# Optimization experiments

Measured on AMD Instinct MI355X. Metric: run time of the kernel, lower is better.

The kernel has to match this reference:

```python
import jax, jax.numpy as jnp
import numpy as np

TOPK = 64  # init kwarg: number of dst routes kept per src node


def setup_inputs() -> dict:
    key = jax.random.key(0)
    ks = jax.random.split(key, 6)
    B, J, K, D, Dd = 4, 4096, 8192, 64, 64  # batch, src_nodes, dst_nodes, src_dim, dst_dim
    val = jax.random.normal(ks[0], (B, J, D), jnp.float32)
    state = jax.random.normal(ks[1], (B, J), jnp.float32)
    dst_state = jax.random.normal(ks[2], (B, K), jnp.float32)
    dst_val = jax.random.normal(ks[3], (B, K, Dd), jnp.float32)
    W_route = jax.random.normal(ks[4], (D, K), jnp.float32) / np.sqrt(D).astype(np.float32)
    W_val = jax.random.normal(ks[5], (D, Dd), jnp.float32) / np.sqrt(D).astype(np.float32)
    return dict(val=val, state=state, dst_state=dst_state, dst_val=dst_val,
                W_route=W_route, W_val=W_val)


def _sparse_routes(logits, topk):
    # top-k indices per src node, scatter a bool mask, masked softmax over dst axis
    _, idx = jax.lax.top_k(logits, topk)              # [B, J, topk]
    B, J, K = logits.shape
    mask = jnp.zeros((B, J, K), dtype=bool)
    mask = mask.at[jnp.arange(B)[:, None, None],
                   jnp.arange(J)[None, :, None], idx].set(True)
    neg = jnp.finfo(logits.dtype).min
    return jax.nn.softmax(jnp.where(mask, logits, neg), axis=-1)


def reference(val, state, dst_state, dst_val, W_route, W_val):
    # route_fn: linear over src val -> logits [B, J, K]
    logits = jnp.einsum('bjd,dk->bjk', val, W_route)
    routes = _sparse_routes(logits, TOPK)             # sparse masked softmax
    projected_val = jnp.einsum('bjd,de->bje', val, W_val)  # val_proj_fn (Linear)
    projected_state = state                            # state_proj_fn = Identity
    sender = jax.nn.softplus(state)                    # state_activation_fn
    weighted = routes * sender[..., None]              # [B, J, K]
    delta_state = jnp.einsum('bjk,bj->bk', weighted, projected_state)
    delta_val = jnp.einsum('bjk,bjd->bkd', weighted, projected_val)
    # merge_mode='add'
    return (dst_state + delta_state, dst_val + delta_val)
```

## Files before the change

### kernel.cpp

```cpp
#include <hip/hip_runtime.h>
#include <math.h>

#define NB 4
#define J 4096
#define KDIM 8192
#define DDIM 64
#define DD 64
#define TOPK 64

#define BM 32
#define THREADS 512
#define THREADS_SEL 256
#define NITER_H 8
#define CAP_H 128
#define GCAP 256
#define OVFCAP 262144

#define KG 128
#define NGRP (KDIM / KG)
#define GLCAP 8192
#define BINROWS 16
#define BINCAP 96
#define CH 128
#define MAXTASK 40960

typedef _Float16 half8_t __attribute__((ext_vector_type(8)));
typedef float f32x16 __attribute__((ext_vector_type(16)));
union H8 { half8_t h; uint4 u; };
__device__ __forceinline__ half8_t as_h8(uint4 v) { H8 x; x.u = v; return x.h; }

__device__ __forceinline__ unsigned f2key(float f) {
  unsigned u = __float_as_uint(f);
  return u ^ (unsigned)(((int)u >> 31) | 0x80000000);
}
__device__ __forceinline__ float key2f(unsigned k) {
  unsigned u = (k & 0x80000000u) ? (k & 0x7FFFFFFFu) : ~k;
  return __uint_as_float(u);
}
__device__ __forceinline__ unsigned wred_maxu(unsigned v) {
  #pragma unroll
  for (int o = 32; o > 0; o >>= 1) { unsigned u = __shfl_xor(v, o, 64); v = u > v ? u : v; }
  return v;
}
__device__ __forceinline__ unsigned wred_minu(unsigned v) {
  #pragma unroll
  for (int o = 32; o > 0; o >>= 1) { unsigned u = __shfl_xor(v, o, 64); v = u < v ? u : v; }
  return v;
}
__device__ __forceinline__ float wred_addf(float v) {
  #pragma unroll
  for (int o = 32; o > 0; o >>= 1) v += __shfl_xor(v, o, 64);
  return v;
}

__global__ void k_prep(const float* __restrict__ W, unsigned* __restrict__ WFh,
                       float* __restrict__ WT)
{
  __shared__ _Float16 lh[64][64];
  __shared__ float lf[64][64];
  const int t = threadIdx.x;
  const int kb = blockIdx.x * 64;
  for (int i = t; i < 4096; i += 256) {
    const int d = i >> 6, c = i & 63;
    const float x = W[(size_t)d * KDIM + kb + c];
    lh[c][d] = (_Float16)x;
    lf[c][d] = x;
  }
  __syncthreads();
  for (int q = t; q < 512; q += 256) {
    const int gt2 = q >> 8, rem = q & 255;
    const int ks = rem >> 6, lane = rem & 63;
    const int c = gt2 * 32 + (lane & 31);
    const int d0 = ks * 16 + (lane >> 5) * 8;
    const int gtile = blockIdx.x * 2 + gt2;
    const size_t off = ((size_t)(gtile * 4 + ks) * 64 + lane) * 4;
    *(uint4*)(WFh + off) = *(const uint4*)&lh[c][d0];
  }
  for (int q = t; q < 1024; q += 256) {
    const int c = q >> 4, d0 = (q & 15) * 4;
    *(float4*)(WT + (size_t)(kb + c) * DDIM + d0) = *(const float4*)&lf[c][d0];
  }
}

__global__ void k_init(const float* __restrict__ dst_state,
                       const float* __restrict__ dst_val,
                       float* __restrict__ out_state, float* __restrict__ out_val)
{
  const size_t i = (size_t)blockIdx.x * blockDim.x + threadIdx.x;
  const size_t stride = (size_t)gridDim.x * blockDim.x;
  const size_t nS = (size_t)NB * KDIM;
  const size_t nV4 = (size_t)NB * KDIM * DD / 4;
  for (size_t q = i; q < nV4; q += stride)
    ((float4*)out_val)[q] = ((const float4*)dst_val)[q];
  for (size_t q = i; q < nS; q += stride)
    out_state[q] = dst_state[q];
}

__global__ __launch_bounds__(THREADS, 4) void k_cand(
    const float* __restrict__ val, const unsigned* __restrict__ WFh,
    const float* __restrict__ W_val, float* __restrict__ pv,
    unsigned short* __restrict__ gidx, unsigned* __restrict__ gcnt,
    float* __restrict__ gtau, unsigned* __restrict__ flags)
{
  __shared__ __align__(16) float val_lds[BM][DDIM + 4];
  __shared__ unsigned short cand_idx[BM][CAP_H];
  __shared__ unsigned have[BM];
  __shared__ float tauF[BM];

  const int t = threadIdx.x;
  const int lane = t & 63;
  const int wv = t >> 6;
  const int hi = lane >> 5;
  const int lane31 = lane & 31;
  const int row0 = blockIdx.x * BM;
  const int h = blockIdx.y;

  {
    const int r = t >> 4, d0 = (t & 15) * 4;
    const float4 v4 = *(const float4*)(val + (size_t)(row0 + r) * DDIM + d0);
    val_lds[r][d0] = v4.x; val_lds[r][d0 + 1] = v4.y;
    val_lds[r][d0 + 2] = v4.z; val_lds[r][d0 + 3] = v4.w;
  }
  __syncthreads();

  if (t < BM) {
    float n2 = 0.f;
    #pragma unroll
    for (int d = 0; d < DDIM; ++d) { const float x = val_lds[t][d]; n2 = fmaf(x, x, n2); }
    tauF[t] = 0.26f * sqrtf(n2);
    have[t] = 0u;
    if (h == 0) gtau[row0 + t] = tauF[t];
  }

  half8_t ah[4];
  {
    const int m = lane31;
    #pragma unroll
    for (int ks = 0; ks < 4; ++ks) {
      const int d0 = ks * 16 + hi * 8;
      #pragma unroll
      for (int j = 0; j < 8; ++j) ah[ks][j] = (_Float16)val_lds[m][d0 + j];
    }
  }
  __syncthreads();

  float taufr[16];
  #pragma unroll
  for (int r = 0; r < 16; ++r) taufr[r] = tauF[(r & 3) + 8 * (r >> 2) + 4 * hi];

  const unsigned* wpBase = WFh + (size_t)(h * 128 + wv * 2) * 1024 + lane * 4;
  const unsigned* wp = wpBase;
  uint4 b0 = *(const uint4*)(wp);        uint4 b1 = *(const uint4*)(wp + 256);
  uint4 b2 = *(const uint4*)(wp + 512);  uint4 b3 = *(const uint4*)(wp + 768);
  uint4 b4 = *(const uint4*)(wp + 1024); uint4 b5 = *(const uint4*)(wp + 1280);
  uint4 b6 = *(const uint4*)(wp + 1536); uint4 b7 = *(const uint4*)(wp + 1792);

  #pragma unroll 1
  for (int it = 0; it < NITER_H; ++it) {
    f32x16 acc0, acc1;
    #pragma unroll
    for (int i = 0; i < 16; ++i) { acc0[i] = 0.f; acc1[i] = 0.f; }
    acc0 = __builtin_amdgcn_mfma_f32_32x32x16_f16(ah[0], as_h8(b0), acc0, 0, 0, 0);
    acc1 = __builtin_amdgcn_mfma_f32_32x32x16_f16(ah[0], as_h8(b4), acc1, 0, 0, 0);
    acc0 = __builtin_amdgcn_mfma_f32_32x32x16_f16(ah[1], as_h8(b1), acc0, 0, 0, 0);
    acc1 = __builtin_amdgcn_mfma_f32_32x32x16_f16(ah[1], as_h8(b5), acc1, 0, 0, 0);
    acc0 = __builtin_amdgcn_mfma_f32_32x32x16_f16(ah[2], as_h8(b2), acc0, 0, 0, 0);
    acc1 = __builtin_amdgcn_mfma_f32_32x32x16_f16(ah[2], as_h8(b6), acc1, 0, 0, 0);
    acc0 = __builtin_amdgcn_mfma_f32_32x32x16_f16(ah[3], as_h8(b3), acc0, 0, 0, 0);
    acc1 = __builtin_amdgcn_mfma_f32_32x32x16_f16(ah[3], as_h8(b7), acc1, 0, 0, 0);

    const unsigned colbase = (unsigned)((h * 128 + it * 16 + wv * 2) * 32 + lane31);

    wp = (it == NITER_H - 1) ? wpBase : wp + 16384;
    b0 = *(const uint4*)(wp);        b1 = *(const uint4*)(wp + 256);
    b2 = *(const uint4*)(wp + 512);  b3 = *(const uint4*)(wp + 768);
    b4 = *(const uint4*)(wp + 1024); b5 = *(const uint4*)(wp + 1280);
    b6 = *(const uint4*)(wp + 1536); b7 = *(const uint4*)(wp + 1792);

    #pragma unroll
    for (int r = 0; r < 16; ++r) {
      const int row = (r & 3) + 8 * (r >> 2) + 4 * hi;
      const float tf = taufr[r];
      if (acc0[r] > tf) {
        const unsigned slot = atomicAdd(&have[row], 1u);
        if (slot < CAP_H) cand_idx[row][slot] = (unsigned short)colbase;
      }
      if (acc1[r] > tf) {
        const unsigned slot = atomicAdd(&have[row], 1u);
        if (slot < CAP_H) cand_idx[row][slot] = (unsigned short)(colbase + 32);
      }
    }
  }

  if (h == 1) {
    const int r = t >> 4, e0 = (t & 15) * 4;
    float a0 = 0.f, a1 = 0.f, a2 = 0.f, a3 = 0.f;
    #pragma unroll 8
    for (int d = 0; d < DDIM; ++d) {
      const float v = val_lds[r][d];
      const float4 w4 = *(const float4*)(W_val + (size_t)d * DD + e0);
      a0 = fmaf(v, w4.x, a0); a1 = fmaf(v, w4.y, a1);
      a2 = fmaf(v, w4.z, a2); a3 = fmaf(v, w4.w, a3);
    }
    *(float4*)(pv + (size_t)(row0 + r) * DD + e0) = make_float4(a0, a1, a2, a3);
  }

  __syncthreads();

  for (int i = t; i < BM * CAP_H; i += THREADS) {
    const int r = i >> 7, s = i & (CAP_H - 1);
    const unsigned hv = have[r];
    const int lim = hv < CAP_H ? (int)hv : CAP_H;
    if (s < lim)
      gidx[(size_t)(row0 + r) * GCAP + h * CAP_H + s] = cand_idx[r][s];
  }
  if (t < BM) {
    const unsigned hv = have[t];
    gcnt[(size_t)(row0 + t) * 2 + h] = hv < CAP_H ? hv : CAP_H;
    if (hv > CAP_H) flags[row0 + t] = 1u;
  }
}

__global__ __launch_bounds__(THREADS_SEL, 4) void k_select(
    const float* __restrict__ val, const float* __restrict__ state,
    const float* __restrict__ WT,
    const unsigned short* __restrict__ gidx, const unsigned* __restrict__ gcnt,
    const float* __restrict__ gtau, unsigned* __restrict__ flags,
    uint2* __restrict__ routes, unsigned* __restrict__ rcnt)
{
  __shared__ float skey[THREADS_SEL / 64][GCAP];
  const int t = threadIdx.x;
  const int lane = t & 63;
  const int wv = t >> 6;
  const int row = blockIdx.x * (THREADS_SEL / 64) + wv;

  if (flags[row]) return;
  const int c0 = (int)gcnt[(size_t)row * 2];
  const int c1 = (int)gcnt[(size_t)row * 2 + 1];
  const int nc = c0 + c1;
  if (nc < TOPK) { if (lane == 0) flags[row] = 1u; return; }
  const float tau = gtau[row];

  const int cq = lane >> 2;
  const int dq = lane & 3;
  float4 v4[4];
  #pragma unroll
  for (int j = 0; j < 4; ++j)
    v4[j] = *(const float4*)(val + (size_t)row * DDIM + j * 16 + dq * 4);

  const unsigned short* grow = gidx + (size_t)row * GCAP;

  unsigned id4[4];
  #pragma unroll
  for (int i = 0; i < 4; ++i) {
    const int s = i * 64 + lane;
    id4[i] = 0xFFFFFFFFu;
    if (s < nc) {
      const int ps = s < c0 ? s : (s - c0 + CAP_H);
      id4[i] = (unsigned)grow[ps];
    }
  }

  for (int s0 = 0; s0 < nc; s0 += 32) {
    const int sA = s0 + cq;
    const int sB = s0 + 16 + cq;
    const bool okA = sA < nc, okB = sB < nc;
    int psA = sA < c0 ? sA : (sA - c0 + CAP_H); if (!okA) psA = 0;
    int psB = sB < c0 ? sB : (sB - c0 + CAP_H); if (!okB) psB = 0;
    const unsigned kkA = (unsigned)grow[psA] & (KDIM - 1);
    const unsigned kkB = (unsigned)grow[psB] & (KDIM - 1);
    const float* wtA = WT + (size_t)kkA * DDIM + dq * 4;
    const float* wtB = WT + (size_t)kkB * DDIM + dq * 4;
    float4 wA[4], wB[4];
    #pragma unroll
    for (int j = 0; j < 4; ++j) wA[j] = *(const float4*)(wtA + j * 16);
    #pragma unroll
    for (int j = 0; j < 4; ++j) wB[j] = *(const float4*)(wtB + j * 16);
    float aA = 0.f, aB = 0.f;
    #pragma unroll
    for (int j = 0; j < 4; ++j) {
      aA = fmaf(v4[j].x, wA[j].x, aA); aA = fmaf(v4[j].y, wA[j].y, aA);
      aA = fmaf(v4[j].z, wA[j].z, aA); aA = fmaf(v4[j].w, wA[j].w, aA);
      aB = fmaf(v4[j].x, wB[j].x, aB); aB = fmaf(v4[j].y, wB[j].y, aB);
      aB = fmaf(v4[j].z, wB[j].z, aB); aB = fmaf(v4[j].w, wB[j].w, aB);
    }
    aA += __shfl_xor(aA, 1, 64); aA += __shfl_xor(aA, 2, 64);
    aB += __shfl_xor(aB, 1, 64); aB += __shfl_xor(aB, 2, 64);
    if (dq == 0) {
      if (okA) skey[wv][sA] = aA;
      if (okB) skey[wv][sB] = aB;
    }
  }
  asm volatile("s_waitcnt lgkmcnt(0)" ::: "memory");
  __builtin_amdgcn_sched_barrier(0);

  unsigned k4[4];
  #pragma unroll
  for (int i = 0; i < 4; ++i) {
    const int s = i * 64 + lane;
    k4[i] = (s < nc) ? f2key(skey[wv][s]) : 0u;
  }
  unsigned lmax = k4[0];
  #pragma unroll
  for (int i = 1; i < 4; ++i) lmax = k4[i] > lmax ? k4[i] : lmax;
  const unsigned kmaxAll = wred_maxu(lmax);
  unsigned klo = f2key(0.99f * tau); if (klo == 0u) klo = 1u;
  unsigned khi = kmaxAll + 1u;
  auto cge4 = [&](unsigned th) {
    int c = 0;
    #pragma unroll
    for (int i = 0; i < 4; ++i) c += __popcll(__ballot(k4[i] >= th));
    return c;
  };
  int cnt = nc;
  while (cnt != TOPK && khi - klo > 1u) {
    const unsigned mid = klo + ((khi - klo) >> 1);
    const int c = cge4(mid);
    if (c >= TOPK) { klo = mid; cnt = c; } else khi = mid;
  }
  const unsigned thr = klo;
  if (key2f(thr) <= 1.006f * tau) {
    if (lane == 0) flags[row] = 1u;
    return;
  }
  unsigned selmask = 0u;
  if (cnt == TOPK) {
    #pragma unroll
    for (int i = 0; i < 4; ++i) if (k4[i] >= thr) selmask |= 1u << i;
  } else {
    #pragma unroll
    for (int i = 0; i < 4; ++i) if (k4[i] > thr) selmask |= 1u << i;
    int tot = 0;
    #pragma unroll
    for (int i = 0; i < 4; ++i) tot += __popcll(__ballot((selmask >> i) & 1));
    int need = TOPK - tot;
    while (need > 0) {
      unsigned best = 0xFFFFFFFFu; int bi = -1;
      #pragma unroll
      for (int i = 0; i < 4; ++i)
        if (k4[i] == thr && !(selmask & (1u << i)) && id4[i] < best) { best = id4[i]; bi = i; }
      const unsigned g = wred_minu(best);
      if (g == 0xFFFFFFFFu) break;
      if (bi >= 0 && best == g) selmask |= 1u << bi;
      --need;
    }
  }
  const float m = key2f(kmaxAll);
  float p[4]; float lsum = 0.f;
  #pragma unroll
  for (int i = 0; i < 4; ++i) {
    p[i] = 0.f;
    if (selmask & (1u << i)) { p[i] = __expf(key2f(k4[i]) - m); lsum += p[i]; }
  }
  lsum = wred_addf(lsum);
  const float st = state[row];
  const float sender = st > 20.f ? st : log1pf(__expf(st));
  const float scale = sender / lsum;
  const unsigned jloc = (unsigned)(row & (J - 1));

  uint2* rrow = routes + (size_t)row * 64;
  int pre = 0;
  #pragma unroll
  for (int i = 0; i < 4; ++i) {
    const bool sel = (selmask >> i) & 1;
    const unsigned long long mball = __ballot(sel);
    const int off = pre + __popcll(mball & ((1ull << lane) - 1ull));
    if (sel)
      rrow[off] = make_uint2(__float_as_uint(p[i] * scale),
                             (id4[i] << 12) | jloc);
    pre += __popcll(mball);
  }
  if (lane == 0) rcnt[row] = (unsigned)pre;
}

__global__ void k_fix(const float* __restrict__ val, const float* __restrict__ state,
                      const float* __restrict__ W, const unsigned* __restrict__ flags,
                      uint2* __restrict__ routes, unsigned* __restrict__ rcnt)
{
  __shared__ unsigned anyf;
  __shared__ unsigned lsk[64][TOPK + 1];
  __shared__ unsigned short lsi[64][TOPK];
  const int t = threadIdx.x;
  const int row = blockIdx.x * 64 + t;
  if (t == 0) anyf = 0u;
  __syncthreads();
  const unsigned f = flags[row];
  if (f) anyf = 1u;
  __syncthreads();
  if (!anyf) return;
  if (!f) return;

  float v[DDIM];
  #pragma unroll
  for (int d = 0; d < DDIM; ++d) v[d] = val[(size_t)row * DDIM + d];
  int m = 0, worst = 0;
  for (int k = 0; k < KDIM; ++k) {
    float acc = 0.f;
    #pragma unroll 8
    for (int d = 0; d < DDIM; ++d) acc = fmaf(v[d], W[(size_t)d * KDIM + k], acc);
    const unsigned key = f2key(acc);
    if (m < TOPK) {
      lsk[t][m] = key; lsi[t][m] = (unsigned short)k; ++m;
      if (m == TOPK) {
        worst = 0;
        for (int q = 1; q < TOPK; ++q)
          if (lsk[t][q] < lsk[t][worst] ||
              (lsk[t][q] == lsk[t][worst] && lsi[t][q] > lsi[t][worst])) worst = q;
      }
    } else if (key > lsk[t][worst]) {
      lsk[t][worst] = key; lsi[t][worst] = (unsigned short)k;
      worst = 0;
      for (int q = 1; q < TOPK; ++q)
        if (lsk[t][q] < lsk[t][worst] ||
            (lsk[t][q] == lsk[t][worst] && lsi[t][q] > lsi[t][worst])) worst = q;
    }
  }
  unsigned km = lsk[t][0];
  for (int q = 1; q < TOPK; ++q) if (lsk[t][q] > km) km = lsk[t][q];
  const float mx = key2f(km);
  float lsum = 0.f;
  for (int q = 0; q < TOPK; ++q) lsum += __expf(key2f(lsk[t][q]) - mx);
  const float st = state[row];
  const float sender = st > 20.f ? st : log1pf(__expf(st));
  const float scale = sender / lsum;
  const unsigned jloc = (unsigned)(row & (J - 1));
  uint2* rrow = routes + (size_t)row * 64;
  for (int q = 0; q < TOPK; ++q) {
    const float w = __expf(key2f(lsk[t][q]) - mx) * scale;
    rrow[q] = make_uint2(__float_as_uint(w), ((unsigned)lsi[t][q] << 12) | jloc);
  }
  rcnt[row] = TOPK;
}

__global__ __launch_bounds__(256, 2) void k_bin(
    const uint2* __restrict__ routes, const unsigned* __restrict__ rcnt,
    unsigned* __restrict__ glcnt, uint2* __restrict__ glist,
    unsigned* __restrict__ ovf_cnt, uint2* __restrict__ ovf)
{
  __shared__ uint2 bins[NGRP][BINCAP];
  __shared__ unsigned bcnt[NGRP];
  __shared__ unsigned bbase[NGRP];
  const int t = threadIdx.x;
  const int lane = t & 63;
  const int wv = t >> 6;
  const int row0 = blockIdx.x * BINROWS;
  const int b = row0 / J;

  for (int i = t; i < NGRP; i += 256) bcnt[i] = 0u;
  __syncthreads();

  for (int i = t; i < BINROWS * 64; i += 256) {
    const int r = i >> 6, s = i & 63;
    unsigned n = rcnt[row0 + r]; if (n > 64u) n = 64u;
    if (s < (int)n) {
      const uint2 e = routes[(size_t)(row0 + r) * 64 + s];
      const unsigned k = e.y >> 12;
      const unsigned g = k >> 7;
      const unsigned slot = atomicAdd(&bcnt[g], 1u);
      if (slot < BINCAP) bins[g][slot] = e;
      else {
        const unsigned op = atomicAdd(ovf_cnt, 1u);
        if (op < (unsigned)OVFCAP)
          ovf[op] = make_uint2(e.x, (((unsigned)b * KDIM + k) << 12) | (e.y & (J - 1)));
      }
    }
  }
  __syncthreads();

  if (t < NGRP) {
    unsigned c = bcnt[t]; if (c > BINCAP) c = BINCAP;
    bcnt[t] = c;
    bbase[t] = c ? atomicAdd(&glcnt[b * NGRP + t], c) : 0u;
  }
  __syncthreads();

  for (int g = wv * 16; g < wv * 16 + 16; ++g) {
    const unsigned c = bcnt[g];
    const unsigned base = bbase[g];
    uint2* dst = glist + (size_t)(b * NGRP + g) * GLCAP;
    for (unsigned i2 = lane; i2 < c; i2 += 64) {
      const unsigned pos = base + i2;
      const uint2 e = bins[g][i2];
      if (pos < GLCAP) dst[pos] = e;
      else {
        const unsigned k = e.y >> 12;
        const unsigned op = atomicAdd(ovf_cnt, 1u);
        if (op < (unsigned)OVFCAP)
          ovf[op] = make_uint2(e.x, (((unsigned)b * KDIM + k) << 12) | (e.y & (J - 1)));
      }
    }
  }
}

__global__ void k_sort(const unsigned* __restrict__ glcnt, const uint2* __restrict__ glist,
                       uint2* __restrict__ glist2, unsigned* __restrict__ ntask,
                       uint2* __restrict__ tasks)
{
  __shared__ unsigned hist[KG];
  __shared__ unsigned offs[KG];
  __shared__ unsigned cur[KG];
  const int t = threadIdx.x;
  const int b = blockIdx.x >> 6;
  const int g = blockIdx.x & (NGRP - 1);
  unsigned n = glcnt[b * NGRP + g]; if (n > (unsigned)GLCAP) n = (unsigned)GLCAP;
  const uint2* src = glist + (size_t)(b * NGRP + g) * GLCAP;
  uint2* dst = glist2 + (size_t)(b * NGRP + g) * GLCAP;

  for (int i = t; i < KG; i += 256) hist[i] = 0u;
  __syncthreads();
  for (unsigned i = t; i < n; i += 256)
    atomicAdd(&hist[(src[i].y >> 12) & (KG - 1)], 1u);
  __syncthreads();
  if (t < KG) offs[t] = hist[t];
  __syncthreads();
  for (int d = 1; d < KG; d <<= 1) {
    unsigned v = 0u;
    if (t < KG && t >= d) v = offs[t - d];
    __syncthreads();
    if (t < KG) offs[t] += v;
    __syncthreads();
  }
  if (t < KG) {
    const unsigned h = hist[t];
    const unsigned base = offs[t] - h;
    cur[t] = base;
    if (h) {
      const unsigned nt = (h + CH - 1) / CH;
      unsigned tbase = atomicAdd(ntask, nt);
      const unsigned bk = (unsigned)b * KDIM + (unsigned)g * KG + (unsigned)t;
      for (unsigned s = 0; s < nt && tbase + s < (unsigned)MAXTASK; ++s) {
        const unsigned st = base + s * CH;
        unsigned ln = h - s * CH; if (ln > (unsigned)CH) ln = CH;
        tasks[tbase + s] = make_uint2(bk, st | (ln << 16));
      }
    }
  }
  __syncthreads();
  for (unsigned i = t; i < n; i += 256) {
    const uint2 e = src[i];
    const unsigned p = atomicAdd(&cur[(e.y >> 12) & (KG - 1)], 1u);
    dst[p] = e;
  }
}

__global__ void k_gather(const unsigned* __restrict__ ntask,
                         const uint2* __restrict__ tasks,
                         const uint2* __restrict__ glist2,
                         const float* __restrict__ pv, const float* __restrict__ state,
                         float* __restrict__ out_state, float* __restrict__ out_val)
{
  const unsigned wid = ((unsigned)blockIdx.x * blockDim.x + threadIdx.x) >> 6;
  const int lane = threadIdx.x & 63;
  unsigned nt = *ntask; if (nt > (unsigned)MAXTASK) nt = (unsigned)MAXTASK;
  if (wid >= nt) return;
  const uint2 tk = tasks[wid];
  const unsigned bk = tk.x;
  const int b = (int)(bk >> 13);
  const unsigned k = bk & (KDIM - 1);
  const unsigned g = k >> 7;
  const unsigned st = tk.y & 0xFFFFu;
  const unsigned n = tk.y >> 16;
  const size_t jbase = (size_t)b * J;
  const uint2* lst = glist2 + (size_t)((unsigned)b * NGRP + g) * GLCAP + st;

  float a0 = 0.f, a1 = 0.f, a2 = 0.f, a3 = 0.f;
  float s0 = 0.f, s1 = 0.f, s2 = 0.f, s3 = 0.f;
  unsigned i = 0;
  for (; i + 4 <= n; i += 4) {
    const uint2 e0 = lst[i + 0], e1 = lst[i + 1], e2 = lst[i + 2], e3 = lst[i + 3];
    const float w0 = __uint_as_float(e0.x), w1 = __uint_as_float(e1.x);
    const float w2 = __uint_as_float(e2.x), w3 = __uint_as_float(e3.x);
    const unsigned j0 = e0.y & (J - 1), j1 = e1.y & (J - 1);
    const unsigned j2 = e2.y & (J - 1), j3 = e3.y & (J - 1);
    a0 = fmaf(w0, pv[(jbase + j0) * DD + lane], a0);
    a1 = fmaf(w1, pv[(jbase + j1) * DD + lane], a1);
    a2 = fmaf(w2, pv[(jbase + j2) * DD + lane], a2);
    a3 = fmaf(w3, pv[(jbase + j3) * DD + lane], a3);
    s0 = fmaf(w0, state[jbase + j0], s0); s1 = fmaf(w1, state[jbase + j1], s1);
    s2 = fmaf(w2, state[jbase + j2], s2); s3 = fmaf(w3, state[jbase + j3], s3);
  }
  for (; i < n; ++i) {
    const uint2 e = lst[i];
    const float w = __uint_as_float(e.x);
    const unsigned j = e.y & (J - 1);
    a0 = fmaf(w, pv[(jbase + j) * DD + lane], a0);
    s0 = fmaf(w, state[jbase + j], s0);
  }
  atomicAdd(&out_val[(size_t)bk * DD + lane], (a0 + a1) + (a2 + a3));
  if (lane == 0) atomicAdd(&out_state[bk], (s0 + s1) + (s2 + s3));
}

__global__ void k_ovf(const unsigned* __restrict__ ovf_cnt, const uint2* __restrict__ ovf,
                      const float* __restrict__ pv, const float* __restrict__ state,
                      float* __restrict__ out_state, float* __restrict__ out_val)
{
  unsigned n = *ovf_cnt;
  if (n > (unsigned)OVFCAP) n = (unsigned)OVFCAP;
  const unsigned wglob = (blockIdx.x * blockDim.x + threadIdx.x) >> 6;
  const int lane = threadIdx.x & 63;
  const unsigned nw = (gridDim.x * blockDim.x) >> 6;
  for (unsigned i = wglob; i < n; i += nw) {
    const uint2 e = ovf[i];
    const float w = __uint_as_float(e.x);
    const unsigned bk = e.y >> 12;
    const unsigned j = e.y & (J - 1);
    const size_t jg = (size_t)(bk >> 13) * J + j;
    atomicAdd(&out_val[(size_t)bk * DD + lane], w * pv[jg * DD + lane]);
    if (lane == 0) atomicAdd(&out_state[bk], w * state[jg]);
  }
}

extern "C" void kernel_launch(void* const* d_in, const int* in_sizes, int n_in,
                              void* d_out, int out_size, void* d_ws, size_t ws_size,
                              hipStream_t stream)
{
  (void)in_sizes; (void)n_in; (void)out_size; (void)ws_size;
  const float* val       = (const float*)d_in[0];
  const float* state     = (const float*)d_in[1];
  const float* dst_state = (const float*)d_in[2];
  const float* dst_val   = (const float*)d_in[3];
  const float* W_route   = (const float*)d_in[4];
  const float* W_val     = (const float*)d_in[5];
  float* out_state = (float*)d_out;
  float* out_val   = out_state + (size_t)NB * KDIM;

  char* p = (char*)d_ws;
  unsigned* rcnt    = (unsigned*)p;  p += (size_t)NB * J * 4;
  unsigned* flags   = (unsigned*)p;  p += (size_t)NB * J * 4;
  unsigned* ovf_cnt = (unsigned*)p;  p += 256;
  unsigned* gcnt    = (unsigned*)p;  p += (size_t)NB * J * 2 * 4;
  unsigned* glcnt   = (unsigned*)p;  p += (size_t)NB * NGRP * 4;
  uint2* tasks      = (uint2*)p;     p += (size_t)MAXTASK * 8;
  float* pv         = (float*)p;     p += (size_t)NB * J * DD * 4;
  unsigned* WFh     = (unsigned*)p;  p += (size_t)KDIM * DDIM * 2;
  float* WT         = (float*)p;     p += (size_t)KDIM * DDIM * 4;
  float* gtau       = (float*)p;     p += (size_t)NB * J * 4;
  unsigned short* gidx = (unsigned short*)p;
  uint2* glist2     = (uint2*)p;     p += (size_t)NB * J * GCAP * 2;
  uint2* routes     = (uint2*)p;     p += (size_t)NB * J * 64 * 8;
  uint2* glist      = (uint2*)p;     p += (size_t)NB * NGRP * GLCAP * 8;
  uint2* ovf        = (uint2*)p;     p += (size_t)OVFCAP * 8;
  unsigned* ntask   = ovf_cnt + 1;

  hipMemsetAsync(rcnt, 0,
                 (size_t)NB * J * 4 + (size_t)NB * J * 4 + 256 +
                 (size_t)NB * J * 2 * 4 + (size_t)NB * NGRP * 4, stream);

  hipLaunchKernelGGL(k_prep, dim3(KDIM / 64), dim3(256), 0, stream, W_route, WFh, WT);
  hipLaunchKernelGGL(k_init, dim3(1024), dim3(256), 0, stream,
                     dst_state, dst_val, out_state, out_val);
  hipLaunchKernelGGL(k_cand, dim3(NB * J / BM, 2), dim3(THREADS), 0, stream,
                     val, WFh, W_val, pv, gidx, gcnt, gtau, flags);
  hipLaunchKernelGGL(k_select, dim3(NB * J / (THREADS_SEL / 64)), dim3(THREADS_SEL),
                     0, stream, val, state, WT, gidx, gcnt, gtau, flags,
                     routes, rcnt);
  hipLaunchKernelGGL(k_fix, dim3(NB * J / 64), dim3(64), 0, stream,
                     val, state, W_route, flags, routes, rcnt);
  hipLaunchKernelGGL(k_bin, dim3(NB * J / BINROWS), dim3(256), 0, stream,
                     routes, rcnt, glcnt, glist, ovf_cnt, ovf);
  hipLaunchKernelGGL(k_sort, dim3(NB * NGRP), dim3(256), 0, stream,
                     glcnt, glist, glist2, ntask, tasks);
  hipLaunchKernelGGL(k_gather, dim3(MAXTASK / 4), dim3(256), 0, stream,
                     ntask, tasks, glist2, pv, state, out_state, out_val);
  hipLaunchKernelGGL(k_ovf, dim3(256), dim3(256), 0, stream,
                     ovf_cnt, ovf, pv, state, out_state, out_val);
}
```

Baseline: 196.7 us.

## Split candidate search into four K segments and merge init and overflow kernels

The candidate-filtering kernel now splits the destination axis into four segments instead of two. This doubles the number of blocks and halves the per-block iteration count, with a smaller per-segment candidate cap, and select maps candidate slots across the four segments. The output init copy is folded into the weight-prep kernel as extra blocks, and the overflow scatter is merged into the gather kernel, removing two launches. Costs include recomputing the threshold and staging val in twice as many blocks, and extra segment-mapping arithmetic in select. Rows whose candidates overflow the smaller cap fall back to the slow fix path more often.

```diff
diff --git a/kernel.cpp b/kernel.cpp
--- a/kernel.cpp
+++ b/kernel.cpp
@@ -11,9 +11,10 @@
 #define BM 32
 #define THREADS 512
 #define THREADS_SEL 256
-#define NITER_H 8
-#define CAP_H 128
-#define GCAP 256
+#define NSEG 4
+#define NITER_S 4
+#define CAP_S 80
+#define GCAPR (NSEG * CAP_S)
 #define OVFCAP 262144
 
 #define KG 128
@@ -54,8 +55,23 @@
 }
 
 __global__ void k_prep(const float* __restrict__ W, unsigned* __restrict__ WFh,
-                       float* __restrict__ WT)
-{
+                       float* __restrict__ WT,
+                       const float* __restrict__ dst_state,
+                       const float* __restrict__ dst_val,
+                       float* __restrict__ out_state, float* __restrict__ out_val)
+{
+  if (blockIdx.x >= KDIM / 64) {
+    const unsigned bid2 = blockIdx.x - KDIM / 64;
+    const size_t i = (size_t)bid2 * 256 + threadIdx.x;
+    const size_t stride = (size_t)1024 * 256;
+    const size_t nS = (size_t)NB * KDIM;
+    const size_t nV4 = (size_t)NB * KDIM * DD / 4;
+    for (size_t q = i; q < nV4; q += stride)
+      ((float4*)out_val)[q] = ((const float4*)dst_val)[q];
+    for (size_t q = i; q < nS; q += stride)
+      out_state[q] = dst_state[q];
+    return;
+  }
   __shared__ _Float16 lh[64][64];
   __shared__ float lf[64][64];
   const int t = threadIdx.x;
@@ -82,20 +98,6 @@
   }
 }
 
-__global__ void k_init(const float* __restrict__ dst_state,
-                       const float* __restrict__ dst_val,
-                       float* __restrict__ out_state, float* __restrict__ out_val)
-{
-  const size_t i = (size_t)blockIdx.x * blockDim.x + threadIdx.x;
-  const size_t stride = (size_t)gridDim.x * blockDim.x;
-  const size_t nS = (size_t)NB * KDIM;
-  const size_t nV4 = (size_t)NB * KDIM * DD / 4;
-  for (size_t q = i; q < nV4; q += stride)
-    ((float4*)out_val)[q] = ((const float4*)dst_val)[q];
-  for (size_t q = i; q < nS; q += stride)
-    out_state[q] = dst_state[q];
-}
-
 __global__ __launch_bounds__(THREADS, 4) void k_cand(
     const float* __restrict__ val, const unsigned* __restrict__ WFh,
     const float* __restrict__ W_val, float* __restrict__ pv,
@@ -103,7 +105,7 @@
     float* __restrict__ gtau, unsigned* __restrict__ flags)
 {
   __shared__ __align__(16) float val_lds[BM][DDIM + 4];
-  __shared__ unsigned short cand_idx[BM][CAP_H];
+  __shared__ unsigned short cand_idx[BM][CAP_S];
   __shared__ unsigned have[BM];
   __shared__ float tauF[BM];
 
@@ -148,7 +150,7 @@
   #pragma unroll
   for (int r = 0; r < 16; ++r) taufr[r] = tauF[(r & 3) + 8 * (r >> 2) + 4 * hi];
 
-  const unsigned* wpBase = WFh + (size_t)(h * 128 + wv * 2) * 1024 + lane * 4;
+  const unsigned* wpBase = WFh + (size_t)(h * 64 + wv * 2) * 1024 + lane * 4;
   const unsigned* wp = wpBase;
   uint4 b0 = *(const uint4*)(wp);        uint4 b1 = *(const uint4*)(wp + 256);
   uint4 b2 = *(const uint4*)(wp + 512);  uint4 b3 = *(const uint4*)(wp + 768);
@@ -156,7 +158,7 @@
   uint4 b6 = *(const uint4*)(wp + 1536); uint4 b7 = *(const uint4*)(wp + 1792);
 
   #pragma unroll 1
-  for (int it = 0; it < NITER_H; ++it) {
+  for (int it = 0; it < NITER_S; ++it) {
     f32x16 acc0, acc1;
     #pragma unroll
     for (int i = 0; i < 16; ++i) { acc0[i] = 0.f; acc1[i] = 0.f; }
@@ -169,9 +171,9 @@
     acc0 = __builtin_amdgcn_mfma_f32_32x32x16_f16(ah[3], as_h8(b3), acc0, 0, 0, 0);
     acc1 = __builtin_amdgcn_mfma_f32_32x32x16_f16(ah[3], as_h8(b7), acc1, 0, 0, 0);
 
-    const unsigned colbase = (unsigned)((h * 128 + it * 16 + wv * 2) * 32 + lane31);
-
-    wp = (it == NITER_H - 1) ? wpBase : wp + 16384;
+    const unsigned colbase = (unsigned)((h * 64 + it * 16 + wv * 2) * 32 + lane31);
+
+    wp = (it == NITER_S - 1) ? wpBase : wp + 16384;
     b0 = *(const uint4*)(wp);        b1 = *(const uint4*)(wp + 256);
     b2 = *(const uint4*)(wp + 512);  b3 = *(const uint4*)(wp + 768);
     b4 = *(const uint4*)(wp + 1024); b5 = *(const uint4*)(wp + 1280);
@@ -183,16 +185,16 @@
       const float tf = taufr[r];
       if (acc0[r] > tf) {
         const unsigned slot = atomicAdd(&have[row], 1u);
-        if (slot < CAP_H) cand_idx[row][slot] = (unsigned short)colbase;
+        if (slot < CAP_S) cand_idx[row][slot] = (unsigned short)colbase;
       }
       if (acc1[r] > tf) {
         const unsigned slot = atomicAdd(&have[row], 1u);
-        if (slot < CAP_H) cand_idx[row][slot] = (unsigned short)(colbase + 32);
+        if (slot < CAP_S) cand_idx[row][slot] = (unsigned short)(colbase + 32);
       }
     }
   }
 
-  if (h == 1) {
+  if (h == 3) {
     const int r = t >> 4, e0 = (t & 15) * 4;
     float a0 = 0.f, a1 = 0.f, a2 = 0.f, a3 = 0.f;
     #pragma unroll 8
@@ -207,17 +209,18 @@
 
   __syncthreads();
 
-  for (int i = t; i < BM * CAP_H; i += THREADS) {
-    const int r = i >> 7, s = i & (CAP_H - 1);
+  #pragma unroll
+  for (int rr = 0; rr < 4; ++rr) {
+    const int r = wv * 4 + rr;
     const unsigned hv = have[r];
-    const int lim = hv < CAP_H ? (int)hv : CAP_H;
-    if (s < lim)
-      gidx[(size_t)(row0 + r) * GCAP + h * CAP_H + s] = cand_idx[r][s];
+    const int lim = hv < CAP_S ? (int)hv : CAP_S;
+    for (int s = lane; s < lim; s += 64)
+      gidx[(size_t)(row0 + r) * GCAPR + h * CAP_S + s] = cand_idx[r][s];
   }
   if (t < BM) {
     const unsigned hv = have[t];
-    gcnt[(size_t)(row0 + t) * 2 + h] = hv < CAP_H ? hv : CAP_H;
-    if (hv > CAP_H) flags[row0 + t] = 1u;
+    gcnt[(size_t)(row0 + t) * NSEG + h] = hv < CAP_S ? hv : CAP_S;
+    if (hv > CAP_S) flags[row0 + t] = 1u;
   }
 }
 
@@ -228,18 +231,27 @@
     const float* __restrict__ gtau, unsigned* __restrict__ flags,
     uint2* __restrict__ routes, unsigned* __restrict__ rcnt)
 {
-  __shared__ float skey[THREADS_SEL / 64][GCAP];
+  __shared__ float skey[THREADS_SEL / 64][256];
   const int t = threadIdx.x;
   const int lane = t & 63;
   const int wv = t >> 6;
   const int row = blockIdx.x * (THREADS_SEL / 64) + wv;
 
   if (flags[row]) return;
-  const int c0 = (int)gcnt[(size_t)row * 2];
-  const int c1 = (int)gcnt[(size_t)row * 2 + 1];
-  const int nc = c0 + c1;
-  if (nc < TOPK) { if (lane == 0) flags[row] = 1u; return; }
+  const unsigned* gc = gcnt + (size_t)row * NSEG;
+  const int c0 = (int)gc[0], c1 = (int)gc[1], c2 = (int)gc[2], c3 = (int)gc[3];
+  const int p1 = c0, p2 = c0 + c1, p3 = c0 + c1 + c2;
+  const int nc = p3 + c3;
+  if (nc < TOPK || nc > 256) { if (lane == 0) flags[row] = 1u; return; }
   const float tau = gtau[row];
+
+  auto mapseg = [&](int s) {
+    int seg = 0, pb = 0;
+    if (s >= p1) { seg = 1; pb = p1; }
+    if (s >= p2) { seg = 2; pb = p2; }
+    if (s >= p3) { seg = 3; pb = p3; }
+    return s - pb + seg * CAP_S;
+  };
 
   const int cq = lane >> 2;
   const int dq = lane & 3;
@@ -248,25 +260,22 @@
   for (int j = 0; j < 4; ++j)
     v4[j] = *(const float4*)(val + (size_t)row * DDIM + j * 16 + dq * 4);
 
-  const unsigned short* grow = gidx + (size_t)row * GCAP;
+  const unsigned short* grow = gidx + (size_t)row * GCAPR;
 
   unsigned id4[4];
   #pragma unroll
   for (int i = 0; i < 4; ++i) {
     const int s = i * 64 + lane;
     id4[i] = 0xFFFFFFFFu;
-    if (s < nc) {
-      const int ps = s < c0 ? s : (s - c0 + CAP_H);
-      id4[i] = (unsigned)grow[ps];
-    }
+    if (s < nc) id4[i] = (unsigned)grow[mapseg(s)];
   }
 
   for (int s0 = 0; s0 < nc; s0 += 32) {
     const int sA = s0 + cq;
     const int sB = s0 + 16 + cq;
     const bool okA = sA < nc, okB = sB < nc;
-    int psA = sA < c0 ? sA : (sA - c0 + CAP_H); if (!okA) psA = 0;
-    int psB = sB < c0 ? sB : (sB - c0 + CAP_H); if (!okB) psB = 0;
+    const int psA = okA ? mapseg(sA) : 0;
+    const int psB = okB ? mapseg(sB) : 0;
     const unsigned kkA = (unsigned)grow[psA] & (KDIM - 1);
     const unsigned kkB = (unsigned)grow[psB] & (KDIM - 1);
     const float* wtA = WT + (size_t)kkA * DDIM + dq * 4;
@@ -547,59 +556,55 @@
                          const uint2* __restrict__ tasks,
                          const uint2* __restrict__ glist2,
                          const float* __restrict__ pv, const float* __restrict__ state,
-                         float* __restrict__ out_state, float* __restrict__ out_val)
+                         float* __restrict__ out_state, float* __restrict__ out_val,
+                         const unsigned* __restrict__ ovf_cnt,
+                         const uint2* __restrict__ ovf)
 {
   const unsigned wid = ((unsigned)blockIdx.x * blockDim.x + threadIdx.x) >> 6;
   const int lane = threadIdx.x & 63;
   unsigned nt = *ntask; if (nt > (unsigned)MAXTASK) nt = (unsigned)MAXTASK;
-  if (wid >= nt) return;
-  const uint2 tk = tasks[wid];
-  const unsigned bk = tk.x;
-  const int b = (int)(bk >> 13);
-  const unsigned k = bk & (KDIM - 1);
-  const unsigned g = k >> 7;
-  const unsigned st = tk.y & 0xFFFFu;
-  const unsigned n = tk.y >> 16;
-  const size_t jbase = (size_t)b * J;
-  const uint2* lst = glist2 + (size_t)((unsigned)b * NGRP + g) * GLCAP + st;
-
-  float a0 = 0.f, a1 = 0.f, a2 = 0.f, a3 = 0.f;
-  float s0 = 0.f, s1 = 0.f, s2 = 0.f, s3 = 0.f;
-  unsigned i = 0;
-  for (; i + 4 <= n; i += 4) {
-    const uint2 e0 = lst[i + 0], e1 = lst[i + 1], e2 = lst[i + 2], e3 = lst[i + 3];
-    const float w0 = __uint_as_float(e0.x), w1 = __uint_as_float(e1.x);
-    const float w2 = __uint_as_float(e2.x), w3 = __uint_as_float(e3.x);
-    const unsigned j0 = e0.y & (J - 1), j1 = e1.y & (J - 1);
-    const unsigned j2 = e2.y & (J - 1), j3 = e3.y & (J - 1);
-    a0 = fmaf(w0, pv[(jbase + j0) * DD + lane], a0);
-    a1 = fmaf(w1, pv[(jbase + j1) * DD + lane], a1);
-    a2 = fmaf(w2, pv[(jbase + j2) * DD + lane], a2);
-    a3 = fmaf(w3, pv[(jbase + j3) * DD + lane], a3);
-    s0 = fmaf(w0, state[jbase + j0], s0); s1 = fmaf(w1, state[jbase + j1], s1);
-    s2 = fmaf(w2, state[jbase + j2], s2); s3 = fmaf(w3, state[jbase + j3], s3);
-  }
-  for (; i < n; ++i) {
-    const uint2 e = lst[i];
-    const float w = __uint_as_float(e.x);
-    const unsigned j = e.y & (J - 1);
-    a0 = fmaf(w, pv[(jbase + j) * DD + lane], a0);
-    s0 = fmaf(w, state[jbase + j], s0);
-  }
-  atomicAdd(&out_val[(size_t)bk * DD + lane], (a0 + a1) + (a2 + a3));
-  if (lane == 0) atomicAdd(&out_state[bk], (s0 + s1) + (s2 + s3));
-}
-
-__global__ void k_ovf(const unsigned* __restrict__ ovf_cnt, const uint2* __restrict__ ovf,
-                      const float* __restrict__ pv, const float* __restrict__ state,
-                      float* __restrict__ out_state, float* __restrict__ out_val)
-{
-  unsigned n = *ovf_cnt;
-  if (n > (unsigned)OVFCAP) n = (unsigned)OVFCAP;
-  const unsigned wglob = (blockIdx.x * blockDim.x + threadIdx.x) >> 6;
-  const int lane = threadIdx.x & 63;
-  const unsigned nw = (gridDim.x * blockDim.x) >> 6;
-  for (unsigned i = wglob; i < n; i += nw) {
+  if (wid < nt) {
+    const uint2 tk = tasks[wid];
+    const unsigned bk = tk.x;
+    const int b = (int)(bk >> 13);
+    const unsigned k = bk & (KDIM - 1);
+    const unsigned g = k >> 7;
+    const unsigned st = tk.y & 0xFFFFu;
+    const unsigned n = tk.y >> 16;
+    const size_t jbase = (size_t)b * J;
+    const uint2* lst = glist2 + (size_t)((unsigned)b * NGRP + g) * GLCAP + st;
+
+    float a0 = 0.f, a1 = 0.f, a2 = 0.f, a3 = 0.f;
+    float s0 = 0.f, s1 = 0.f, s2 = 0.f, s3 = 0.f;
+    unsigned i = 0;
+    for (; i + 4 <= n; i += 4) {
+      const uint2 e0 = lst[i + 0], e1 = lst[i + 1], e2 = lst[i + 2], e3 = lst[i + 3];
+      const float w0 = __uint_as_float(e0.x), w1 = __uint_as_float(e1.x);
+      const float w2 = __uint_as_float(e2.x), w3 = __uint_as_float(e3.x);
+      const unsigned j0 = e0.y & (J - 1), j1 = e1.y & (J - 1);
+      const unsigned j2 = e2.y & (J - 1), j3 = e3.y & (J - 1);
+      a0 = fmaf(w0, pv[(jbase + j0) * DD + lane], a0);
+      a1 = fmaf(w1, pv[(jbase + j1) * DD + lane], a1);
+      a2 = fmaf(w2, pv[(jbase + j2) * DD + lane], a2);
+      a3 = fmaf(w3, pv[(jbase + j3) * DD + lane], a3);
+      s0 = fmaf(w0, state[jbase + j0], s0); s1 = fmaf(w1, state[jbase + j1], s1);
+      s2 = fmaf(w2, state[jbase + j2], s2); s3 = fmaf(w3, state[jbase + j3], s3);
+    }
+    for (; i < n; ++i) {
+      const uint2 e = lst[i];
+      const float w = __uint_as_float(e.x);
+      const unsigned j = e.y & (J - 1);
+      a0 = fmaf(w, pv[(jbase + j) * DD + lane], a0);
+      s0 = fmaf(w, state[jbase + j], s0);
+    }
+    atomicAdd(&out_val[(size_t)bk * DD + lane], (a0 + a1) + (a2 + a3));
+    if (lane == 0) atomicAdd(&out_state[bk], (s0 + s1) + (s2 + s3));
+  }
+
+  unsigned novf = *ovf_cnt;
+  if (novf > (unsigned)OVFCAP) novf = (unsigned)OVFCAP;
+  const unsigned nw = ((unsigned)gridDim.x * blockDim.x) >> 6;
+  for (unsigned i = wid; i < novf; i += nw) {
     const uint2 e = ovf[i];
     const float w = __uint_as_float(e.x);
     const unsigned bk = e.y >> 12;
@@ -628,7 +633,7 @@
   unsigned* rcnt    = (unsigned*)p;  p += (size_t)NB * J * 4;
   unsigned* flags   = (unsigned*)p;  p += (size_t)NB * J * 4;
   unsigned* ovf_cnt = (unsigned*)p;  p += 256;
-  unsigned* gcnt    = (unsigned*)p;  p += (size_t)NB * J * 2 * 4;
+  unsigned* gcnt    = (unsigned*)p;  p += (size_t)NB * J * NSEG * 4;
   unsigned* glcnt   = (unsigned*)p;  p += (size_t)NB * NGRP * 4;
   uint2* tasks      = (uint2*)p;     p += (size_t)MAXTASK * 8;
   float* pv         = (float*)p;     p += (size_t)NB * J * DD * 4;
@@ -636,7 +641,7 @@
   float* WT         = (float*)p;     p += (size_t)KDIM * DDIM * 4;
   float* gtau       = (float*)p;     p += (size_t)NB * J * 4;
   unsigned short* gidx = (unsigned short*)p;
-  uint2* glist2     = (uint2*)p;     p += (size_t)NB * J * GCAP * 2;
+  uint2* glist2     = (uint2*)p;     p += (size_t)NB * J * GCAPR * 2;
   uint2* routes     = (uint2*)p;     p += (size_t)NB * J * 64 * 8;
   uint2* glist      = (uint2*)p;     p += (size_t)NB * NGRP * GLCAP * 8;
   uint2* ovf        = (uint2*)p;     p += (size_t)OVFCAP * 8;
@@ -644,12 +649,11 @@
 
   hipMemsetAsync(rcnt, 0,
                  (size_t)NB * J * 4 + (size_t)NB * J * 4 + 256 +
-                 (size_t)NB * J * 2 * 4 + (size_t)NB * NGRP * 4, stream);
-
-  hipLaunchKernelGGL(k_prep, dim3(KDIM / 64), dim3(256), 0, stream, W_route, WFh, WT);
-  hipLaunchKernelGGL(k_init, dim3(1024), dim3(256), 0, stream,
-                     dst_state, dst_val, out_state, out_val);
-  hipLaunchKernelGGL(k_cand, dim3(NB * J / BM, 2), dim3(THREADS), 0, stream,
+                 (size_t)NB * J * NSEG * 4 + (size_t)NB * NGRP * 4, stream);
+
+  hipLaunchKernelGGL(k_prep, dim3(KDIM / 64 + 1024), dim3(256), 0, stream,
+                     W_route, WFh, WT, dst_state, dst_val, out_state, out_val);
+  hipLaunchKernelGGL(k_cand, dim3(NB * J / BM, NSEG), dim3(THREADS), 0, stream,
                      val, WFh, W_val, pv, gidx, gcnt, gtau, flags);
   hipLaunchKernelGGL(k_select, dim3(NB * J / (THREADS_SEL / 64)), dim3(THREADS_SEL),
                      0, stream, val, state, WT, gidx, gcnt, gtau, flags,
@@ -661,7 +665,6 @@
   hipLaunchKernelGGL(k_sort, dim3(NB * NGRP), dim3(256), 0, stream,
                      glcnt, glist, glist2, ntask, tasks);
   hipLaunchKernelGGL(k_gather, dim3(MAXTASK / 4), dim3(256), 0, stream,
-                     ntask, tasks, glist2, pv, state, out_state, out_val);
-  hipLaunchKernelGGL(k_ovf, dim3(256), dim3(256), 0, stream,
-                     ovf_cnt, ovf, pv, state, out_state, out_val);
-}
+                     ntask, tasks, glist2, pv, state, out_state, out_val,
+                     ovf_cnt, ovf);
+}
```

Measured after the change: 198.7 us. No clear change (+1.0%).
